# Optimization experiments

Measured on AMD Instinct MI355X. Metric: run time of the kernel, lower is better.

## Reference

```python
import jax, jax.numpy as jnp
import numpy as np

C = 64          # residual channels
N_LAYERS = 30
MAX_STEPS = 200
SQRT2 = 2.0 ** 0.5


def _conv1d(x, W, b, dilation=1, pad=0):
    # x: [B, Cin, T], W: [Cout, Cin, K], b: [Cout]
    y = jax.lax.conv_general_dilated(
        x, W, window_strides=(1,), padding=[(pad, pad)],
        rhs_dilation=(dilation,), dimension_numbers=('NCH', 'OIH', 'NCH'))
    return y + b[None, :, None]


def _silu(x):
    return x * jax.nn.sigmoid(x)


def _emb_table():
    steps = jnp.arange(MAX_STEPS, dtype=jnp.float32)[:, None]      # [200,1]
    dims = jnp.arange(64, dtype=jnp.float32)[None, :]              # [1,64]
    t = steps * 10.0 ** (dims * 4.0 / 63.0)                        # [200,64]
    return jnp.concatenate([jnp.sin(t), jnp.cos(t)], axis=1)       # [200,128]


def setup_inputs() -> dict:
    key = jax.random.key(0)
    ks = jax.random.split(key, 20)
    B, T = 4, 16384
    f32 = jnp.float32
    inp = {
        'audio': jax.random.normal(ks[0], (B, 1, T), dtype=f32),
        'diffusion_step': jax.random.randint(ks[1], (B,), 0, MAX_STEPS),
        # input projection Conv1d(1, 64, 1)
        'in_W': jax.random.normal(ks[2], (C, 1, 1), f32) * 1.0,
        'in_b': jax.random.normal(ks[3], (C,), f32) * 0.01,
        # diffusion embedding MLP 128->512->512
        'p1_W': jax.random.normal(ks[4], (512, 128), f32) * (1.0 / np.sqrt(128)),
        'p1_b': jnp.zeros((512,), f32),
        'p2_W': jax.random.normal(ks[5], (512, 512), f32) * (1.0 / np.sqrt(512)),
        'p2_b': jnp.zeros((512,), f32),
        # per-layer params (stacked over 30 layers)
        'dw_W': jax.random.normal(ks[6], (N_LAYERS, 2 * C, C, 3), f32) * (1.0 / np.sqrt(3 * C)),
        'dw_b': jnp.zeros((N_LAYERS, 2 * C), f32),
        'dp_W': jax.random.normal(ks[7], (N_LAYERS, C, 512), f32) * (1.0 / np.sqrt(512)),
        'dp_b': jnp.zeros((N_LAYERS, C), f32),
        'op_W': jax.random.normal(ks[8], (N_LAYERS, 2 * C, C, 1), f32) * (1.0 / np.sqrt(C)),
        'op_b': jnp.zeros((N_LAYERS, 2 * C), f32),
        # skip projection Conv1d(64,64,1)
        'sk_W': jax.random.normal(ks[9], (C, C, 1), f32) * (1.0 / np.sqrt(C)),
        'sk_b': jnp.zeros((C,), f32),
        # output projection Conv1d(64,1,1), weight zero-init like original
        'out_W': jnp.zeros((1, C, 1), f32),
        'out_b': jax.random.normal(ks[10], (1,), f32) * 0.01,
    }
    return inp


def reference(audio, diffusion_step, in_W, in_b, p1_W, p1_b, p2_W, p2_b,
              dw_W, dw_b, dp_W, dp_b, op_W, op_b, sk_W, sk_b, out_W, out_b):
    x = jax.nn.relu(_conv1d(audio, in_W, in_b))                    # [B,64,T]
    # diffusion embedding
    t = _emb_table()[diffusion_step]                               # [B,128]
    t = _silu(t @ p1_W.T + p1_b)                                   # [B,512]
    t = _silu(t @ p2_W.T + p2_b)                                   # [B,512]
    skip = None
    for i in range(N_LAYERS):
        d = 2 ** (i % 10)
        cond = (t @ dp_W[i].T + dp_b[i])[:, :, None]               # [B,64,1]
        y = _conv1d(x + cond, dw_W[i], dw_b[i], dilation=d, pad=d) # [B,128,T]
        gate, filt = y[:, :C], y[:, C:]
        y = jax.nn.sigmoid(gate) * jnp.tanh(filt)                  # [B,64,T]
        y = _conv1d(y, op_W[i], op_b[i])                           # [B,128,T]
        residual, sk = y[:, :C], y[:, C:]
        x = (x + residual) / SQRT2
        skip = sk if skip is None else skip + sk
    x = skip / np.sqrt(float(N_LAYERS)).astype(np.float32)
    x = jax.nn.relu(_conv1d(x, sk_W, sk_b))
    return _conv1d(x, out_W, out_b)                                # [B,1,T]
```

## Files before the change

### kernel.cpp

```cpp
#include <hip/hip_runtime.h>
#include <math.h>

#define C 64
#define NL 30
#define T 16384
#define B 4

typedef __bf16 bf16_t;
typedef __bf16 bf16x8 __attribute__((ext_vector_type(8)));
typedef __bf16 bf16x4 __attribute__((ext_vector_type(4)));
typedef float f32x4 __attribute__((ext_vector_type(4)));

typedef const __attribute__((address_space(1))) unsigned int glb_u32;
typedef __attribute__((address_space(3))) unsigned int lds_u32;

constexpr float INV_SQRT2   = 0.70710678118654752440f;
constexpr float INV_SQRT_NL = 0.18257418583505537115f;

__device__ __forceinline__ float fsig(float x) {
    return __builtin_amdgcn_rcpf(1.f + __builtin_amdgcn_exp2f(-1.44269504089f * x));
}
__device__ __forceinline__ float ftanh(float x) {
    return fmaf(2.f, __builtin_amdgcn_rcpf(1.f + __builtin_amdgcn_exp2f(-2.88539008178f * x)), -1.f);
}
__device__ __forceinline__ int swz(int off) { return off ^ ((off >> 3) & 0x70); }

__global__ void pack_weights(const float* __restrict__ dw_W,
                             const float* __restrict__ op_W,
                             const float* __restrict__ sk_W,
                             bf16_t* __restrict__ convpk,
                             bf16_t* __restrict__ oppk,
                             bf16_t* __restrict__ skpk) {
    int idx = blockIdx.x * 256 + threadIdx.x;
    const int ndw = NL * 128 * 192;
    const int nop = NL * 128 * 64;
    if (idx < ndw) {
        int k = idx % 192; int r = idx / 192;
        int oc = r % 128;  int l = r / 128;
        int tap = k >> 6, ic = k & 63;
        convpk[idx] = (bf16_t)dw_W[((l * 128 + oc) * 64 + ic) * 3 + tap];
    } else if (idx < ndw + nop) {
        oppk[idx - ndw] = (bf16_t)op_W[idx - ndw];
    } else if (idx < ndw + nop + 4096) {
        int j = idx - ndw - nop;
        skpk[j] = (bf16_t)(sk_W[j] * INV_SQRT_NL);
    }
}

__global__ void cond_embp1(const int* __restrict__ step,
                           const float* __restrict__ p1_W, const float* __restrict__ p1_b,
                           float* __restrict__ h1out) {
    __shared__ float e[128];
    __shared__ float red[256];
    int b = blockIdx.x, blk = blockIdx.y, tid = threadIdx.x;
    int s = step[b];
    if (tid < 128) {
        int d = tid & 63;
        float tf = (float)s * powf(10.f, (float)d * 4.f / 63.f);
        double td = (double)tf;
        e[tid] = (tid < 64) ? (float)sin(td) : (float)cos(td);
    }
    __syncthreads();
    int ol = tid >> 2, q = tid & 3;
    int o = blk * 64 + ol;
    const float4* wr = (const float4*)(p1_W + o * 128 + q * 32);
    const float4* ev = (const float4*)(e + q * 32);
    float a = 0.f;
    #pragma unroll
    for (int j = 0; j < 8; ++j) {
        float4 wv = wr[j]; float4 xv = ev[j];
        a = fmaf(wv.x, xv.x, a); a = fmaf(wv.y, xv.y, a);
        a = fmaf(wv.z, xv.z, a); a = fmaf(wv.w, xv.w, a);
    }
    red[tid] = a;
    __syncthreads();
    if (q == 0) {
        float v = red[tid] + red[tid + 1] + red[tid + 2] + red[tid + 3] + p1_b[o];
        h1out[b * 512 + o] = v / (1.f + expf(-v));
    }
}

__global__ void cond_p2(const float* __restrict__ h1,
                        const float* __restrict__ p2_W, const float* __restrict__ p2_b,
                        float* __restrict__ h2out) {
    __shared__ float red[256];
    int b = blockIdx.x, blk = blockIdx.y, tid = threadIdx.x;
    int ol = tid >> 2, q = tid & 3;
    int o = blk * 64 + ol;
    const float4* wr = (const float4*)(p2_W + o * 512 + q * 128);
    const float4* hv = (const float4*)(h1 + b * 512 + q * 128);
    float a = 0.f;
    #pragma unroll 8
    for (int j = 0; j < 32; ++j) {
        float4 wv = wr[j]; float4 xv = hv[j];
        a = fmaf(wv.x, xv.x, a); a = fmaf(wv.y, xv.y, a);
        a = fmaf(wv.z, xv.z, a); a = fmaf(wv.w, xv.w, a);
    }
    red[tid] = a;
    __syncthreads();
    if (q == 0) {
        float v = red[tid] + red[tid + 1] + red[tid + 2] + red[tid + 3] + p2_b[o];
        h2out[b * 512 + o] = v / (1.f + expf(-v));
    }
}

__global__ void cond_stage2b(const float* __restrict__ h2,
                             const float* __restrict__ dp_W, const float* __restrict__ dp_b,
                             const bf16_t* __restrict__ convpk,
                             const float* __restrict__ dw_b,
                             float* __restrict__ bias2) {
    __shared__ float red[256];
    __shared__ float cond_s[64];
    int l = blockIdx.x, b = blockIdx.y;
    int tid = threadIdx.x;
    {
        int o = tid >> 2, q = tid & 3;
        const float4* wr = (const float4*)(dp_W + ((size_t)l * C + o) * 512 + q * 128);
        const float4* h = (const float4*)(h2 + b * 512 + q * 128);
        float a = 0.f;
        #pragma unroll 8
        for (int j = 0; j < 32; ++j) {
            float4 wv = wr[j]; float4 hv = h[j];
            a = fmaf(wv.x, hv.x, a); a = fmaf(wv.y, hv.y, a);
            a = fmaf(wv.z, hv.z, a); a = fmaf(wv.w, hv.w, a);
        }
        red[tid] = a;
        __syncthreads();
        if (q == 0)
            cond_s[o] = red[tid] + red[tid + 1] + red[tid + 2] + red[tid + 3] + dp_b[l * C + o];
    }
    __syncthreads();
    int oc = tid & 127, kh = tid >> 7;
    const bf16_t* wr = convpk + ((size_t)l * 128 + oc) * 192 + kh * 96;
    float a = kh ? 0.f : dw_b[l * 128 + oc];
    #pragma unroll
    for (int j = 0; j < 96; ++j)
        a = fmaf((float)wr[j], cond_s[(kh * 96 + j) & 63], a);
    __syncthreads();
    red[tid] = a;
    __syncthreads();
    if (tid < 128)
        bias2[(l * B + b) * 128 + tid] = red[tid] + red[tid + 128];
}

__global__ void in_conv(const float* __restrict__ audio,
                        const float* __restrict__ in_W, const float* __restrict__ in_b,
                        bf16_t* __restrict__ x) {
    int idx = blockIdx.x * 256 + threadIdx.x;
    int cb = idx & 7;
    int t = (idx >> 3) & (T - 1);
    int b = idx >> 17;
    float av = audio[b * T + t];
    bf16x8 o;
    #pragma unroll
    for (int j = 0; j < 8; ++j) {
        int c = cb * 8 + j;
        o[j] = (bf16_t)fmaxf(fmaf(in_W[c], av, in_b[c]), 0.f);
    }
    *(bf16x8*)(x + ((size_t)b * T + t) * 64 + cb * 8) = o;
}

__global__ __launch_bounds__(256) void layer_kernel(
    const bf16_t* __restrict__ x_in, bf16_t* __restrict__ x_out, bf16_t* __restrict__ skip,
    const bf16_t* __restrict__ convpk, const bf16_t* __restrict__ oppk,
    const float* __restrict__ bias2, const float* __restrict__ op_b,
    const bf16_t* __restrict__ zpage,
    int layer, int dil, int first)
{
    __shared__ uint4 smem_u[2048];
    char* sm = (char*)smem_u;

    int tid = threadIdx.x;
    int w = __builtin_amdgcn_readfirstlane(tid >> 6);
    int l = tid & 63;
    int lr = l & 15;
    int g = l >> 4;
    int b = blockIdx.y;
    int bid = blockIdx.x;
    int tile = ((bid & 7) << 4) + (bid >> 3);
    int tbase = tile * 128;
    const bf16_t* xb = x_in + (size_t)b * T * 64;

    bf16x8 cA[2][6];
    const bf16_t* cw = convpk + (size_t)layer * 128 * 192;
    #pragma unroll
    for (int mf = 0; mf < 2; ++mf)
        #pragma unroll
        for (int kf = 0; kf < 6; ++kf)
            cA[mf][kf] = *(const bf16x8*)(cw + (mf * 64 + w * 16 + lr) * 192 + kf * 32 + g * 8);
    bf16x8 oA[2][2];
    const bf16_t* ow = oppk + (size_t)layer * 128 * 64;
    #pragma unroll
    for (int mf = 0; mf < 2; ++mf)
        #pragma unroll
        for (int kf = 0; kf < 2; ++kf)
            oA[mf][kf] = *(const bf16x8*)(ow + (mf * 64 + w * 16 + lr) * 64 + kf * 32 + g * 8);
    f32x4 bC[2], bO[2];
    const float* b2 = bias2 + (layer * B + b) * 128;
    const float* ob = op_b + layer * 2 * C;
    #pragma unroll
    for (int mf = 0; mf < 2; ++mf)
        #pragma unroll
        for (int r = 0; r < 4; ++r) {
            bC[mf][r] = b2[mf * 64 + w * 16 + g * 4 + r];
            bO[mf][r] = ob[mf * 64 + w * 16 + g * 4 + r];
        }

    size_t bb = (size_t)b * T * 64;

    for (int st = 0; st < 2; ++st) {
        int t0 = tbase + st * 64;

        #pragma unroll
        for (int it = 0; it < 6; ++it) {
            int qq = it * 256 + tid;
            int slice = qq >> 9, row = (qq >> 3) & 63, c16 = qq & 7;
            int ts = t0 + row + (slice - 1) * dil;
            int c16s = c16 ^ (row & 7);
            const bf16_t* src = ((unsigned)ts < (unsigned)T)
                ? (xb + (size_t)ts * 64 + c16s * 8)
                : (zpage + c16s * 8);
            __builtin_amdgcn_global_load_lds((glb_u32*)src,
                (lds_u32*)(sm + it * 4096 + w * 1024), 16, 0, 0);
        }
        __syncthreads();

        f32x4 acc[2][4];
        #pragma unroll
        for (int mf = 0; mf < 2; ++mf)
            #pragma unroll
            for (int nf = 0; nf < 4; ++nf) acc[mf][nf] = bC[mf];
        #pragma unroll
        for (int kf = 0; kf < 6; ++kf) {
            int tap = kf >> 1;
            int kc = (kf & 1) * 32;
            bf16x8 Bf[4];
            #pragma unroll
            for (int nf = 0; nf < 4; ++nf) {
                int off = tap * 8192 + (nf * 16 + lr) * 128 + (kc + g * 8) * 2;
                Bf[nf] = *(const bf16x8*)(sm + swz(off));
            }
            #pragma unroll
            for (int mf = 0; mf < 2; ++mf)
                #pragma unroll
                for (int nf = 0; nf < 4; ++nf)
                    acc[mf][nf] = __builtin_amdgcn_mfma_f32_16x16x32_bf16(
                        cA[mf][kf], Bf[nf], acc[mf][nf], 0, 0, 0);
        }

        #pragma unroll
        for (int nf = 0; nf < 4; ++nf) {
            union { bf16_t hh[4]; uint2 u; } zp;
            #pragma unroll
            for (int r = 0; r < 4; ++r)
                zp.hh[r] = (bf16_t)(fsig(acc[0][nf][r]) * ftanh(acc[1][nf][r]));
            int off = 24576 + (nf * 16 + lr) * 128 + (w * 16 + g * 4) * 2;
            *(uint2*)(sm + swz(off)) = zp.u;
        }
        __syncthreads();

        f32x4 acc2[2][4];
        #pragma unroll
        for (int mf = 0; mf < 2; ++mf)
            #pragma unroll
            for (int nf = 0; nf < 4; ++nf) acc2[mf][nf] = bO[mf];
        #pragma unroll
        for (int kf = 0; kf < 2; ++kf) {
            bf16x8 Zf[4];
            #pragma unroll
            for (int nf = 0; nf < 4; ++nf) {
                int off = 24576 + (nf * 16 + lr) * 128 + (kf * 32 + g * 8) * 2;
                Zf[nf] = *(const bf16x8*)(sm + swz(off));
            }
            #pragma unroll
            for (int mf = 0; mf < 2; ++mf)
                #pragma unroll
                for (int nf = 0; nf < 4; ++nf)
                    acc2[mf][nf] = __builtin_amdgcn_mfma_f32_16x16x32_bf16(
                        oA[mf][kf], Zf[nf], acc2[mf][nf], 0, 0, 0);
        }

        #pragma unroll
        for (int nf = 0; nf < 4; ++nf) {
            int t = t0 + nf * 16 + lr;
            int c0 = w * 16 + g * 4;
            int xoff = 8192 + (nf * 16 + lr) * 128 + c0 * 2;
            bf16x4 xv = *(const bf16x4*)(sm + swz(xoff));
            bf16x4 ro, so;
            bf16_t* sp = skip + bb + (size_t)t * 64 + c0;
            if (first) {
                #pragma unroll
                for (int r = 0; r < 4; ++r) {
                    ro[r] = (bf16_t)(((float)xv[r] + acc2[0][nf][r]) * INV_SQRT2);
                    so[r] = (bf16_t)acc2[1][nf][r];
                }
            } else {
                bf16x4 sv = *(const bf16x4*)sp;
                #pragma unroll
                for (int r = 0; r < 4; ++r) {
                    ro[r] = (bf16_t)(((float)xv[r] + acc2[0][nf][r]) * INV_SQRT2);
                    so[r] = (bf16_t)((float)sv[r] + acc2[1][nf][r]);
                }
            }
            *(bf16x4*)(x_out + bb + (size_t)t * 64 + c0) = ro;
            *(bf16x4*)sp = so;
        }
        if (st == 0) __syncthreads();
    }
}

template<int D1, int D2, int YOFF, int NYR, int XOFF, int NXR>
__global__ __launch_bounds__(256) void fused_pair(
    const bf16_t* __restrict__ x_in, bf16_t* __restrict__ x_out,
    bf16_t* __restrict__ skip,
    const bf16_t* __restrict__ convpk, const bf16_t* __restrict__ oppk,
    const float* __restrict__ bias2, const float* __restrict__ op_b,
    const bf16_t* __restrict__ zpage, int layerA, int first)
{
    extern __shared__ char sm[];
    constexpr int NYF = NYR / 16;
    constexpr int CF  = YOFF / 16;
    constexpr int YS  = NXR * 128;
    constexpr int ZS  = YS + NYR * 128;

    int tid = threadIdx.x;
    int w = __builtin_amdgcn_readfirstlane(tid >> 6);
    int l = tid & 63, lr = l & 15, g = l >> 4;
    int bid = blockIdx.x;
    int tile = ((bid & 7) << 5) + (bid >> 3);
    int b = blockIdx.y;
    int t0 = tile * 64;
    size_t bb = (size_t)b * T * 64;
    const bf16_t* xb = x_in + bb;
    int c0 = w * 16 + g * 4;

    #pragma unroll
    for (int r = 0; r < NXR / 32; ++r) {
        int row = r * 32 + (tid >> 3), c16 = tid & 7;
        int ts = t0 - XOFF + row;
        int c16s = c16 ^ (row & 7);
        const bf16_t* src = ((unsigned)ts < (unsigned)T)
            ? (xb + (size_t)ts * 64 + c16s * 8)
            : (zpage + c16s * 8);
        __builtin_amdgcn_global_load_lds((glb_u32*)src,
            (lds_u32*)(sm + r * 4096 + w * 1024), 16, 0, 0);
    }

    float skr[16];
    #pragma unroll
    for (int i = 0; i < 16; ++i) skr[i] = 0.f;

    bf16x8 cA[2][6];
    {
        const bf16_t* cw = convpk + (size_t)layerA * 128 * 192;
        #pragma unroll
        for (int mf = 0; mf < 2; ++mf)
            #pragma unroll
            for (int kf = 0; kf < 6; ++kf)
                cA[mf][kf] = *(const bf16x8*)(cw + (mf * 64 + w * 16 + lr) * 192 + kf * 32 + g * 8);
    }
    bf16x8 oA[2][2];
    {
        const bf16_t* ow = oppk + (size_t)layerA * 128 * 64;
        #pragma unroll
        for (int mf = 0; mf < 2; ++mf)
            #pragma unroll
            for (int kf = 0; kf < 2; ++kf)
                oA[mf][kf] = *(const bf16x8*)(ow + (mf * 64 + w * 16 + lr) * 64 + kf * 32 + g * 8);
    }
    f32x4 bC[2], bO[2];
    {
        const float* b2 = bias2 + (layerA * B + b) * 128;
        const float* ob = op_b + layerA * 2 * C;
        #pragma unroll
        for (int mf = 0; mf < 2; ++mf)
            #pragma unroll
            for (int r = 0; r < 4; ++r) {
                bC[mf][r] = b2[mf * 64 + c0 + r];
                bO[mf][r] = ob[mf * 64 + c0 + r];
            }
    }
    __syncthreads();

    f32x4 acc[2][NYF];
    #pragma unroll
    for (int mf = 0; mf < 2; ++mf)
        #pragma unroll
        for (int nf = 0; nf < NYF; ++nf) acc[mf][nf] = bC[mf];
    #pragma unroll
    for (int kf = 0; kf < 6; ++kf) {
        int tap = kf >> 1;
        int kc = (kf & 1) * 32;
        bf16x8 Bf[NYF];
        #pragma unroll
        for (int nf = 0; nf < NYF; ++nf) {
            int ix = (nf * 16 + lr) + (XOFF - YOFF) + (tap - 1) * D1;
            Bf[nf] = *(const bf16x8*)(sm + swz(ix * 128 + (kc + g * 8) * 2));
        }
        #pragma unroll
        for (int mf = 0; mf < 2; ++mf)
            #pragma unroll
            for (int nf = 0; nf < NYF; ++nf)
                acc[mf][nf] = __builtin_amdgcn_mfma_f32_16x16x32_bf16(
                    cA[mf][kf], Bf[nf], acc[mf][nf], 0, 0, 0);
    }

    #pragma unroll
    for (int nf = 0; nf < NYF; ++nf) {
        union { bf16_t hh[4]; uint2 u; } zp;
        #pragma unroll
        for (int r = 0; r < 4; ++r)
            zp.hh[r] = (bf16_t)(fsig(acc[0][nf][r]) * ftanh(acc[1][nf][r]));
        int off = ZS + (nf * 16 + lr) * 128 + c0 * 2;
        *(uint2*)(sm + swz(off)) = zp.u;
    }
    __syncthreads();

    {
        f32x4 acc2[2][NYF];
        #pragma unroll
        for (int mf = 0; mf < 2; ++mf)
            #pragma unroll
            for (int nf = 0; nf < NYF; ++nf) acc2[mf][nf] = bO[mf];
        #pragma unroll
        for (int kf = 0; kf < 2; ++kf) {
            bf16x8 Zf[NYF];
            #pragma unroll
            for (int nf = 0; nf < NYF; ++nf) {
                int off = ZS + (nf * 16 + lr) * 128 + (kf * 32 + g * 8) * 2;
                Zf[nf] = *(const bf16x8*)(sm + swz(off));
            }
            #pragma unroll
            for (int mf = 0; mf < 2; ++mf)
                #pragma unroll
                for (int nf = 0; nf < NYF; ++nf)
                    acc2[mf][nf] = __builtin_amdgcn_mfma_f32_16x16x32_bf16(
                        oA[mf][kf], Zf[nf], acc2[mf][nf], 0, 0, 0);
        }
        #pragma unroll
        for (int nf = 0; nf < NYF; ++nf) {
            int iy = nf * 16 + lr;
            int ta = t0 - YOFF + iy;
            bool inr = ((unsigned)ta < (unsigned)T);
            int ixc = iy + (XOFF - YOFF);
            bf16x4 xv = *(const bf16x4*)(sm + swz(ixc * 128 + c0 * 2));
            bf16x4 yo;
            #pragma unroll
            for (int r = 0; r < 4; ++r) {
                float yv = ((float)xv[r] + acc2[0][nf][r]) * INV_SQRT2;
                yo[r] = inr ? (bf16_t)yv : (bf16_t)0.f;
                if (nf >= CF && nf < CF + 4)
                    skr[(nf - CF) * 4 + r] += acc2[1][nf][r];
            }
            *(bf16x4*)(sm + swz(YS + iy * 128 + c0 * 2)) = yo;
        }
    }

    int layerB = layerA + 1;
    bf16x8 cB[2][6];
    {
        const bf16_t* cw = convpk + (size_t)layerB * 128 * 192;
        #pragma unroll
        for (int mf = 0; mf < 2; ++mf)
            #pragma unroll
            for (int kf = 0; kf < 6; ++kf)
                cB[mf][kf] = *(const bf16x8*)(cw + (mf * 64 + w * 16 + lr) * 192 + kf * 32 + g * 8);
    }
    bf16x8 oB[2][2];
    {
        const bf16_t* ow = oppk + (size_t)layerB * 128 * 64;
        #pragma unroll
        for (int mf = 0; mf < 2; ++mf)
            #pragma unroll
            for (int kf = 0; kf < 2; ++kf)
                oB[mf][kf] = *(const bf16x8*)(ow + (mf * 64 + w * 16 + lr) * 64 + kf * 32 + g * 8);
    }
    f32x4 bCB[2], bOB[2];
    {
        const float* b2 = bias2 + (layerB * B + b) * 128;
        const float* ob = op_b + layerB * 2 * C;
        #pragma unroll
        for (int mf = 0; mf < 2; ++mf)
            #pragma unroll
            for (int r = 0; r < 4; ++r) {
                bCB[mf][r] = b2[mf * 64 + c0 + r];
                bOB[mf][r] = ob[mf * 64 + c0 + r];
            }
    }
    __syncthreads();

    f32x4 accB[2][4];
    #pragma unroll
    for (int mf = 0; mf < 2; ++mf)
        #pragma unroll
        for (int nf = 0; nf < 4; ++nf) accB[mf][nf] = bCB[mf];
    #pragma unroll
    for (int kf = 0; kf < 6; ++kf) {
        int tap = kf >> 1;
        int kc = (kf & 1) * 32;
        bf16x8 Bf[4];
        #pragma unroll
        for (int nf = 0; nf < 4; ++nf) {
            int jy = (nf * 16 + lr) + YOFF + (tap - 1) * D2;
            Bf[nf] = *(const bf16x8*)(sm + swz(YS + jy * 128 + (kc + g * 8) * 2));
        }
        #pragma unroll
        for (int mf = 0; mf < 2; ++mf)
            #pragma unroll
            for (int nf = 0; nf < 4; ++nf)
                accB[mf][nf] = __builtin_amdgcn_mfma_f32_16x16x32_bf16(
                    cB[mf][kf], Bf[nf], accB[mf][nf], 0, 0, 0);
    }

    #pragma unroll
    for (int nf = 0; nf < 4; ++nf) {
        union { bf16_t hh[4]; uint2 u; } zp;
        #pragma unroll
        for (int r = 0; r < 4; ++r)
            zp.hh[r] = (bf16_t)(fsig(accB[0][nf][r]) * ftanh(accB[1][nf][r]));
        int off = ZS + (nf * 16 + lr) * 128 + c0 * 2;
        *(uint2*)(sm + swz(off)) = zp.u;
    }
    __syncthreads();

    f32x4 acc2B[2][4];
    #pragma unroll
    for (int mf = 0; mf < 2; ++mf)
        #pragma unroll
        for (int nf = 0; nf < 4; ++nf) acc2B[mf][nf] = bOB[mf];
    #pragma unroll
    for (int kf = 0; kf < 2; ++kf) {
        bf16x8 Zf[4];
        #pragma unroll
        for (int nf = 0; nf < 4; ++nf) {
            int off = ZS + (nf * 16 + lr) * 128 + (kf * 32 + g * 8) * 2;
            Zf[nf] = *(const bf16x8*)(sm + swz(off));
        }
        #pragma unroll
        for (int mf = 0; mf < 2; ++mf)
            #pragma unroll
            for (int nf = 0; nf < 4; ++nf)
                acc2B[mf][nf] = __builtin_amdgcn_mfma_f32_16x16x32_bf16(
                    oB[mf][kf], Zf[nf], acc2B[mf][nf], 0, 0, 0);
    }
    #pragma unroll
    for (int nf = 0; nf < 4; ++nf) {
        int it = nf * 16 + lr;
        int t = t0 + it;
        int jyc = it + YOFF;
        bf16x4 yv = *(const bf16x4*)(sm + swz(YS + jyc * 128 + c0 * 2));
        bf16x4 ro, so;
        bf16_t* sp = skip + bb + (size_t)t * 64 + c0;
        if (first) {
            #pragma unroll
            for (int r = 0; r < 4; ++r) {
                ro[r] = (bf16_t)(((float)yv[r] + acc2B[0][nf][r]) * INV_SQRT2);
                so[r] = (bf16_t)(skr[nf * 4 + r] + acc2B[1][nf][r]);
            }
        } else {
            bf16x4 sv = *(const bf16x4*)sp;
            #pragma unroll
            for (int r = 0; r < 4; ++r) {
                ro[r] = (bf16_t)(((float)yv[r] + acc2B[0][nf][r]) * INV_SQRT2);
                so[r] = (bf16_t)((float)sv[r] + skr[nf * 4 + r] + acc2B[1][nf][r]);
            }
        }
        *(bf16x4*)(x_out + bb + (size_t)t * 64 + c0) = ro;
        *(bf16x4*)sp = so;
    }
}

__global__ __launch_bounds__(256) void final_kernel(
    const bf16_t* __restrict__ skip, const bf16_t* __restrict__ skpk,
    const float* __restrict__ sk_b,
    const float* __restrict__ out_W, const float* __restrict__ out_b,
    float* __restrict__ out)
{
    __shared__ uint4 tile_u[512];
    __shared__ float part[16][66];
    unsigned char* sm = (unsigned char*)tile_u;
    int tid = threadIdx.x;
    int w = __builtin_amdgcn_readfirstlane(tid >> 6);
    int l = tid & 63, lr = l & 15, g = l >> 4;
    int bid = blockIdx.x;
    int tile = ((bid & 7) << 5) + (bid >> 3);
    int b = blockIdx.y, t0 = tile * 64;
    const bf16_t* sb = skip + (size_t)b * T * 64;

    #pragma unroll
    for (int it = 0; it < 2; ++it) {
        int q = it * 256 + tid;
        int row = q >> 3, c16 = q & 7;
        uint4 val = *(const uint4*)(sb + (size_t)(t0 + row) * 64 + c16 * 8);
        *(uint4*)(sm + swz(row * 128 + c16 * 16)) = val;
    }

    bf16x8 aS[2];
    #pragma unroll
    for (int kf = 0; kf < 2; ++kf)
        aS[kf] = *(const bf16x8*)(skpk + (w * 16 + lr) * 64 + kf * 32 + g * 8);
    f32x4 acc[4];
    #pragma unroll
    for (int nf = 0; nf < 4; ++nf)
        #pragma unroll
        for (int r = 0; r < 4; ++r) acc[nf][r] = sk_b[w * 16 + g * 4 + r];
    __syncthreads();

    #pragma unroll
    for (int kf = 0; kf < 2; ++kf) {
        bf16x8 Bf[4];
        #pragma unroll
        for (int nf = 0; nf < 4; ++nf) {
            int off = (nf * 16 + lr) * 128 + (kf * 32 + g * 8) * 2;
            Bf[nf] = *(const bf16x8*)(sm + swz(off));
        }
        #pragma unroll
        for (int nf = 0; nf < 4; ++nf)
            acc[nf] = __builtin_amdgcn_mfma_f32_16x16x32_bf16(aS[kf], Bf[nf], acc[nf], 0, 0, 0);
    }

    #pragma unroll
    for (int nf = 0; nf < 4; ++nf) {
        float o = 0.f;
        #pragma unroll
        for (int r = 0; r < 4; ++r)
            o = fmaf(out_W[w * 16 + g * 4 + r], fmaxf(acc[nf][r], 0.f), o);
        part[w * 4 + g][nf * 16 + lr] = o;
    }
    __syncthreads();
    if (tid < 64) {
        float o = out_b[0];
        #pragma unroll
        for (int j = 0; j < 16; ++j) o += part[j][tid];
        out[(size_t)b * T + t0 + tid] = o;
    }
}

extern "C" void kernel_launch(void* const* d_in, const int* in_sizes, int n_in,
                              void* d_out, int out_size, void* d_ws, size_t ws_size,
                              hipStream_t stream) {
    const float* audio = (const float*)d_in[0];
    const int*   dstep = (const int*)d_in[1];
    const float* in_W  = (const float*)d_in[2];
    const float* in_b  = (const float*)d_in[3];
    const float* p1_W  = (const float*)d_in[4];
    const float* p1_b  = (const float*)d_in[5];
    const float* p2_W  = (const float*)d_in[6];
    const float* p2_b  = (const float*)d_in[7];
    const float* dw_W  = (const float*)d_in[8];
    const float* dw_b  = (const float*)d_in[9];
    const float* dp_W  = (const float*)d_in[10];
    const float* dp_b  = (const float*)d_in[11];
    const float* op_W  = (const float*)d_in[12];
    const float* op_b  = (const float*)d_in[13];
    const float* sk_W  = (const float*)d_in[14];
    const float* sk_b  = (const float*)d_in[15];
    const float* out_W = (const float*)d_in[16];
    const float* out_b = (const float*)d_in[17];

    float* ws = (float*)d_ws;
    const size_t NXE = (size_t)B * T * 64;
    float* h1    = ws;
    float* h2    = h1 + B * 512;
    float* bias2 = h2 + B * 512;
    float* zpg   = bias2 + NL * B * 128;
    bf16_t* xA   = (bf16_t*)(zpg + 128);
    bf16_t* xB   = xA + NXE;
    bf16_t* skip = xB + NXE;
    bf16_t* convpk = skip + NXE;
    bf16_t* oppk   = convpk + (size_t)NL * 128 * 192;
    bf16_t* skpk   = oppk + (size_t)NL * 128 * 64;

    hipMemsetAsync(zpg, 0, 512, stream);
    hipLaunchKernelGGL(pack_weights, dim3(3856), dim3(256), 0, stream,
                       dw_W, op_W, sk_W, convpk, oppk, skpk);
    hipLaunchKernelGGL(cond_embp1, dim3(B, 8), dim3(256), 0, stream,
                       dstep, p1_W, p1_b, h1);
    hipLaunchKernelGGL(cond_p2, dim3(B, 8), dim3(256), 0, stream,
                       h1, p2_W, p2_b, h2);
    hipLaunchKernelGGL(cond_stage2b, dim3(NL, B), dim3(256), 0, stream,
                       h2, dp_W, dp_b, convpk, dw_b, bias2);
    hipLaunchKernelGGL(in_conv, dim3(B * T * 8 / 256), dim3(256), 0, stream,
                       audio, in_W, in_b, xA);

    bf16_t* bufs[2] = { xA, xB };
    int cur = 0;
    const bf16_t* zpgc = (const bf16_t*)zpg;
    for (int dec = 0; dec < 3; ++dec) {
        int base = dec * 10;
        hipLaunchKernelGGL((fused_pair<1, 2, 16, 96, 32, 128>),
                           dim3(T / 64, B), dim3(256), 40960, stream,
                           bufs[cur], bufs[cur ^ 1], skip, convpk, oppk,
                           bias2, op_b, zpgc, base + 0, (dec == 0) ? 1 : 0);
        cur ^= 1;
        hipLaunchKernelGGL((fused_pair<4, 8, 16, 96, 32, 128>),
                           dim3(T / 64, B), dim3(256), 40960, stream,
                           bufs[cur], bufs[cur ^ 1], skip, convpk, oppk,
                           bias2, op_b, zpgc, base + 2, 0);
        cur ^= 1;
        hipLaunchKernelGGL((fused_pair<16, 32, 32, 128, 48, 160>),
                           dim3(T / 64, B), dim3(256), 53248, stream,
                           bufs[cur], bufs[cur ^ 1], skip, convpk, oppk,
                           bias2, op_b, zpgc, base + 4, 0);
        cur ^= 1;
        for (int j = 6; j < 10; ++j) {
            int dil = 1 << j;
            hipLaunchKernelGGL(layer_kernel, dim3(T / 128, B), dim3(256), 0, stream,
                               bufs[cur], bufs[cur ^ 1], skip, convpk, oppk,
                               bias2, op_b, zpgc, base + j, dil, 0);
            cur ^= 1;
        }
    }
    hipLaunchKernelGGL(final_kernel, dim3(T / 64, B), dim3(256), 0, stream,
                       skip, skpk, sk_b, out_W, out_b, (float*)d_out);
}
```

Baseline: 467.7 us.

## Fuse input conv into first layer pair and retile single-layer kernel

```diff
diff --git a/kernel.cpp b/kernel.cpp
--- a/kernel.cpp
+++ b/kernel.cpp
@@ -143,24 +143,7 @@
         bias2[(l * B + b) * 128 + tid] = red[tid] + red[tid + 128];
 }
 
-__global__ void in_conv(const float* __restrict__ audio,
-                        const float* __restrict__ in_W, const float* __restrict__ in_b,
-                        bf16_t* __restrict__ x) {
-    int idx = blockIdx.x * 256 + threadIdx.x;
-    int cb = idx & 7;
-    int t = (idx >> 3) & (T - 1);
-    int b = idx >> 17;
-    float av = audio[b * T + t];
-    bf16x8 o;
-    #pragma unroll
-    for (int j = 0; j < 8; ++j) {
-        int c = cb * 8 + j;
-        o[j] = (bf16_t)fmaxf(fmaf(in_W[c], av, in_b[c]), 0.f);
-    }
-    *(bf16x8*)(x + ((size_t)b * T + t) * 64 + cb * 8) = o;
-}
-
-__global__ __launch_bounds__(256) void layer_kernel(
+__global__ __launch_bounds__(256, 4) void layer_kernel(
     const bf16_t* __restrict__ x_in, bf16_t* __restrict__ x_out, bf16_t* __restrict__ skip,
     const bf16_t* __restrict__ convpk, const bf16_t* __restrict__ oppk,
     const float* __restrict__ bias2, const float* __restrict__ op_b,
@@ -177,9 +160,23 @@
     int g = l >> 4;
     int b = blockIdx.y;
     int bid = blockIdx.x;
-    int tile = ((bid & 7) << 4) + (bid >> 3);
-    int tbase = tile * 128;
+    int tile = ((bid & 7) << 5) + (bid >> 3);
+    int t0 = tile * 64;
     const bf16_t* xb = x_in + (size_t)b * T * 64;
+    size_t bb = (size_t)b * T * 64;
+
+    #pragma unroll
+    for (int it = 0; it < 6; ++it) {
+        int qq = it * 256 + tid;
+        int slice = qq >> 9, row = (qq >> 3) & 63, c16 = qq & 7;
+        int ts = t0 + row + (slice - 1) * dil;
+        int c16s = c16 ^ (row & 7);
+        const bf16_t* src = ((unsigned)ts < (unsigned)T)
+            ? (xb + (size_t)ts * 64 + c16s * 8)
+            : (zpage + c16s * 8);
+        __builtin_amdgcn_global_load_lds((glb_u32*)src,
+            (lds_u32*)(sm + it * 4096 + w * 1024), 16, 0, 0);
+    }
 
     bf16x8 cA[2][6];
     const bf16_t* cw = convpk + (size_t)layer * 128 * 192;
@@ -188,6 +185,37 @@
         #pragma unroll
         for (int kf = 0; kf < 6; ++kf)
             cA[mf][kf] = *(const bf16x8*)(cw + (mf * 64 + w * 16 + lr) * 192 + kf * 32 + g * 8);
+    f32x4 bC[2];
+    const float* b2 = bias2 + (layer * B + b) * 128;
+    #pragma unroll
+    for (int mf = 0; mf < 2; ++mf)
+        #pragma unroll
+        for (int r = 0; r < 4; ++r) bC[mf][r] = b2[mf * 64 + w * 16 + g * 4 + r];
+    __syncthreads();
+
+    f32x4 acc[2][4];
+    #pragma unroll
+    for (int mf = 0; mf < 2; ++mf)
+        #pragma unroll
+        for (int nf = 0; nf < 4; ++nf) acc[mf][nf] = bC[mf];
+    #pragma unroll
+    for (int kf = 0; kf < 6; ++kf) {
+        int tap = kf >> 1;
+        int kc = (kf & 1) * 32;
+        bf16x8 Bf[4];
+        #pragma unroll
+        for (int nf = 0; nf < 4; ++nf) {
+            int off = tap * 8192 + (nf * 16 + lr) * 128 + (kc + g * 8) * 2;
+            Bf[nf] = *(const bf16x8*)(sm + swz(off));
+        }
+        #pragma unroll
+        for (int mf = 0; mf < 2; ++mf)
+            #pragma unroll
+            for (int nf = 0; nf < 4; ++nf)
+                acc[mf][nf] = __builtin_amdgcn_mfma_f32_16x16x32_bf16(
+                    cA[mf][kf], Bf[nf], acc[mf][nf], 0, 0, 0);
+    }
+
     bf16x8 oA[2][2];
     const bf16_t* ow = oppk + (size_t)layer * 128 * 64;
     #pragma unroll
@@ -195,127 +223,82 @@
         #pragma unroll
         for (int kf = 0; kf < 2; ++kf)
             oA[mf][kf] = *(const bf16x8*)(ow + (mf * 64 + w * 16 + lr) * 64 + kf * 32 + g * 8);
-    f32x4 bC[2], bO[2];
-    const float* b2 = bias2 + (layer * B + b) * 128;
+    f32x4 bO[2];
     const float* ob = op_b + layer * 2 * C;
     #pragma unroll
     for (int mf = 0; mf < 2; ++mf)
         #pragma unroll
-        for (int r = 0; r < 4; ++r) {
-            bC[mf][r] = b2[mf * 64 + w * 16 + g * 4 + r];
-            bO[mf][r] = ob[mf * 64 + w * 16 + g * 4 + r];
-        }
-
-    size_t bb = (size_t)b * T * 64;
-
-    for (int st = 0; st < 2; ++st) {
-        int t0 = tbase + st * 64;
-
-        #pragma unroll
-        for (int it = 0; it < 6; ++it) {
-            int qq = it * 256 + tid;
-            int slice = qq >> 9, row = (qq >> 3) & 63, c16 = qq & 7;
-            int ts = t0 + row + (slice - 1) * dil;
-            int c16s = c16 ^ (row & 7);
-            const bf16_t* src = ((unsigned)ts < (unsigned)T)
-                ? (xb + (size_t)ts * 64 + c16s * 8)
-                : (zpage + c16s * 8);
-            __builtin_amdgcn_global_load_lds((glb_u32*)src,
-                (lds_u32*)(sm + it * 4096 + w * 1024), 16, 0, 0);
-        }
-        __syncthreads();
-
-        f32x4 acc[2][4];
-        #pragma unroll
-        for (int mf = 0; mf < 2; ++mf)
-            #pragma unroll
-            for (int nf = 0; nf < 4; ++nf) acc[mf][nf] = bC[mf];
-        #pragma unroll
-        for (int kf = 0; kf < 6; ++kf) {
-            int tap = kf >> 1;
-            int kc = (kf & 1) * 32;
-            bf16x8 Bf[4];
-            #pragma unroll
-            for (int nf = 0; nf < 4; ++nf) {
-                int off = tap * 8192 + (nf * 16 + lr) * 128 + (kc + g * 8) * 2;
-                Bf[nf] = *(const bf16x8*)(sm + swz(off));
-            }
-            #pragma unroll
-            for (int mf = 0; mf < 2; ++mf)
-                #pragma unroll
-                for (int nf = 0; nf < 4; ++nf)
-                    acc[mf][nf] = __builtin_amdgcn_mfma_f32_16x16x32_bf16(
-                        cA[mf][kf], Bf[nf], acc[mf][nf], 0, 0, 0);
-        }
-
+        for (int r = 0; r < 4; ++r) bO[mf][r] = ob[mf * 64 + w * 16 + g * 4 + r];
+
+    #pragma unroll
+    for (int nf = 0; nf < 4; ++nf) {
+        union { bf16_t hh[4]; uint2 u; } zp;
+        #pragma unroll
+        for (int r = 0; r < 4; ++r)
+            zp.hh[r] = (bf16_t)(fsig(acc[0][nf][r]) * ftanh(acc[1][nf][r]));
+        int off = 24576 + (nf * 16 + lr) * 128 + (w * 16 + g * 4) * 2;
+        *(uint2*)(sm + swz(off)) = zp.u;
+    }
+    __syncthreads();
+
+    f32x4 acc2[2][4];
+    #pragma unroll
+    for (int mf = 0; mf < 2; ++mf)
+        #pragma unroll
+        for (int nf = 0; nf < 4; ++nf) acc2[mf][nf] = bO[mf];
+    #pragma unroll
+    for (int kf = 0; kf < 2; ++kf) {
+        bf16x8 Zf[4];
         #pragma unroll
         for (int nf = 0; nf < 4; ++nf) {
-            union { bf16_t hh[4]; uint2 u; } zp;
-            #pragma unroll
-            for (int r = 0; r < 4; ++r)
-                zp.hh[r] = (bf16_t)(fsig(acc[0][nf][r]) * ftanh(acc[1][nf][r]));
-            int off = 24576 + (nf * 16 + lr) * 128 + (w * 16 + g * 4) * 2;
-            *(uint2*)(sm + swz(off)) = zp.u;
-        }
-        __syncthreads();
-
-        f32x4 acc2[2][4];
-        #pragma unroll
-        for (int mf = 0; mf < 2; ++mf)
-            #pragma unroll
-            for (int nf = 0; nf < 4; ++nf) acc2[mf][nf] = bO[mf];
-        #pragma unroll
-        for (int kf = 0; kf < 2; ++kf) {
-            bf16x8 Zf[4];
-            #pragma unroll
-            for (int nf = 0; nf < 4; ++nf) {
-                int off = 24576 + (nf * 16 + lr) * 128 + (kf * 32 + g * 8) * 2;
-                Zf[nf] = *(const bf16x8*)(sm + swz(off));
-            }
-            #pragma unroll
-            for (int mf = 0; mf < 2; ++mf)
-                #pragma unroll
-                for (int nf = 0; nf < 4; ++nf)
-                    acc2[mf][nf] = __builtin_amdgcn_mfma_f32_16x16x32_bf16(
-                        oA[mf][kf], Zf[nf], acc2[mf][nf], 0, 0, 0);
-        }
-
-        #pragma unroll
-        for (int nf = 0; nf < 4; ++nf) {
-            int t = t0 + nf * 16 + lr;
-            int c0 = w * 16 + g * 4;
-            int xoff = 8192 + (nf * 16 + lr) * 128 + c0 * 2;
-            bf16x4 xv = *(const bf16x4*)(sm + swz(xoff));
-            bf16x4 ro, so;
-            bf16_t* sp = skip + bb + (size_t)t * 64 + c0;
-            if (first) {
-                #pragma unroll
-                for (int r = 0; r < 4; ++r) {
-                    ro[r] = (bf16_t)(((float)xv[r] + acc2[0][nf][r]) * INV_SQRT2);
-                    so[r] = (bf16_t)acc2[1][nf][r];
-                }
-            } else {
-                bf16x4 sv = *(const bf16x4*)sp;
-                #pragma unroll
-                for (int r = 0; r < 4; ++r) {
-                    ro[r] = (bf16_t)(((float)xv[r] + acc2[0][nf][r]) * INV_SQRT2);
-                    so[r] = (bf16_t)((float)sv[r] + acc2[1][nf][r]);
-                }
-            }
-            *(bf16x4*)(x_out + bb + (size_t)t * 64 + c0) = ro;
-            *(bf16x4*)sp = so;
-        }
-        if (st == 0) __syncthreads();
-    }
-}
-
-template<int D1, int D2, int YOFF, int NYR, int XOFF, int NXR>
+            int off = 24576 + (nf * 16 + lr) * 128 + (kf * 32 + g * 8) * 2;
+            Zf[nf] = *(const bf16x8*)(sm + swz(off));
+        }
+        #pragma unroll
+        for (int mf = 0; mf < 2; ++mf)
+            #pragma unroll
+            for (int nf = 0; nf < 4; ++nf)
+                acc2[mf][nf] = __builtin_amdgcn_mfma_f32_16x16x32_bf16(
+                    oA[mf][kf], Zf[nf], acc2[mf][nf], 0, 0, 0);
+    }
+
+    #pragma unroll
+    for (int nf = 0; nf < 4; ++nf) {
+        int t = t0 + nf * 16 + lr;
+        int c0 = w * 16 + g * 4;
+        int xoff = 8192 + (nf * 16 + lr) * 128 + c0 * 2;
+        bf16x4 xv = *(const bf16x4*)(sm + swz(xoff));
+        bf16x4 ro, so;
+        bf16_t* sp = skip + bb + (size_t)t * 64 + c0;
+        if (first) {
+            #pragma unroll
+            for (int r = 0; r < 4; ++r) {
+                ro[r] = (bf16_t)(((float)xv[r] + acc2[0][nf][r]) * INV_SQRT2);
+                so[r] = (bf16_t)acc2[1][nf][r];
+            }
+        } else {
+            bf16x4 sv = *(const bf16x4*)sp;
+            #pragma unroll
+            for (int r = 0; r < 4; ++r) {
+                ro[r] = (bf16_t)(((float)xv[r] + acc2[0][nf][r]) * INV_SQRT2);
+                so[r] = (bf16_t)((float)sv[r] + acc2[1][nf][r]);
+            }
+        }
+        *(bf16x4*)(x_out + bb + (size_t)t * 64 + c0) = ro;
+        *(bf16x4*)sp = so;
+    }
+}
+
+template<int D1, int D2, int YOFF, int NYR, int XOFF, int NXR, int FROMAUD>
 __global__ __launch_bounds__(256) void fused_pair(
     const bf16_t* __restrict__ x_in, bf16_t* __restrict__ x_out,
     bf16_t* __restrict__ skip,
     const bf16_t* __restrict__ convpk, const bf16_t* __restrict__ oppk,
     const float* __restrict__ bias2, const float* __restrict__ op_b,
-    const bf16_t* __restrict__ zpage, int layerA, int first)
+    const bf16_t* __restrict__ zpage,
+    const float* __restrict__ audio,
+    const float* __restrict__ in_W, const float* __restrict__ in_b,
+    int layerA, int first)
 {
     extern __shared__ char sm[];
     constexpr int NYF = NYR / 16;
@@ -334,16 +317,38 @@
     const bf16_t* xb = x_in + bb;
     int c0 = w * 16 + g * 4;
 
-    #pragma unroll
-    for (int r = 0; r < NXR / 32; ++r) {
-        int row = r * 32 + (tid >> 3), c16 = tid & 7;
-        int ts = t0 - XOFF + row;
-        int c16s = c16 ^ (row & 7);
-        const bf16_t* src = ((unsigned)ts < (unsigned)T)
-            ? (xb + (size_t)ts * 64 + c16s * 8)
-            : (zpage + c16s * 8);
-        __builtin_amdgcn_global_load_lds((glb_u32*)src,
-            (lds_u32*)(sm + r * 4096 + w * 1024), 16, 0, 0);
+    if constexpr (FROMAUD) {
+        #pragma unroll
+        for (int r = 0; r < NXR / 32; ++r) {
+            int q = r * 256 + tid;
+            int row = q >> 3, c16 = q & 7;
+            int ts = t0 - XOFF + row;
+            bf16x8 o;
+            if ((unsigned)ts < (unsigned)T) {
+                float av = audio[(size_t)b * T + ts];
+                #pragma unroll
+                for (int j = 0; j < 8; ++j) {
+                    int c = c16 * 8 + j;
+                    o[j] = (bf16_t)fmaxf(fmaf(in_W[c], av, in_b[c]), 0.f);
+                }
+            } else {
+                #pragma unroll
+                for (int j = 0; j < 8; ++j) o[j] = (bf16_t)0.f;
+            }
+            *(bf16x8*)(sm + swz(row * 128 + c16 * 16)) = o;
+        }
+    } else {
+        #pragma unroll
+        for (int r = 0; r < NXR / 32; ++r) {
+            int row = r * 32 + (tid >> 3), c16 = tid & 7;
+            int ts = t0 - XOFF + row;
+            int c16s = c16 ^ (row & 7);
+            const bf16_t* src = ((unsigned)ts < (unsigned)T)
+                ? (xb + (size_t)ts * 64 + c16s * 8)
+                : (zpage + c16s * 8);
+            __builtin_amdgcn_global_load_lds((glb_u32*)src,
+                (lds_u32*)(sm + r * 4096 + w * 1024), 16, 0, 0);
+        }
     }
 
     float skr[16];
@@ -680,32 +685,37 @@
                        h1, p2_W, p2_b, h2);
     hipLaunchKernelGGL(cond_stage2b, dim3(NL, B), dim3(256), 0, stream,
                        h2, dp_W, dp_b, convpk, dw_b, bias2);
-    hipLaunchKernelGGL(in_conv, dim3(B * T * 8 / 256), dim3(256), 0, stream,
-                       audio, in_W, in_b, xA);
 
     bf16_t* bufs[2] = { xA, xB };
     int cur = 0;
     const bf16_t* zpgc = (const bf16_t*)zpg;
     for (int dec = 0; dec < 3; ++dec) {
         int base = dec * 10;
-        hipLaunchKernelGGL((fused_pair<1, 2, 16, 96, 32, 128>),
+        if (dec == 0) {
+            hipLaunchKernelGGL((fused_pair<1, 2, 16, 96, 32, 128, 1>),
+                               dim3(T / 64, B), dim3(256), 40960, stream,
+                               bufs[cur], bufs[cur ^ 1], skip, convpk, oppk,
+                               bias2, op_b, zpgc, audio, in_W, in_b, 0, 1);
+        } else {
+            hipLaunchKernelGGL((fused_pair<1, 2, 16, 96, 32, 128, 0>),
+                               dim3(T / 64, B), dim3(256), 40960, stream,
+                               bufs[cur], bufs[cur ^ 1], skip, convpk, oppk,
+                               bias2, op_b, zpgc, audio, in_W, in_b, base + 0, 0);
+        }
+        cur ^= 1;
+        hipLaunchKernelGGL((fused_pair<4, 8, 16, 96, 32, 128, 0>),
                            dim3(T / 64, B), dim3(256), 40960, stream,
                            bufs[cur], bufs[cur ^ 1], skip, convpk, oppk,
-                           bias2, op_b, zpgc, base + 0, (dec == 0) ? 1 : 0);
+                           bias2, op_b, zpgc, audio, in_W, in_b, base + 2, 0);
         cur ^= 1;
-        hipLaunchKernelGGL((fused_pair<4, 8, 16, 96, 32, 128>),
-                           dim3(T / 64, B), dim3(256), 40960, stream,
-                           bufs[cur], bufs[cur ^ 1], skip, convpk, oppk,
-                           bias2, op_b, zpgc, base + 2, 0);
-        cur ^= 1;
-        hipLaunchKernelGGL((fused_pair<16, 32, 32, 128, 48, 160>),
+        hipLaunchKernelGGL((fused_pair<16, 32, 32, 128, 48, 160, 0>),
                            dim3(T / 64, B), dim3(256), 53248, stream,
                            bufs[cur], bufs[cur ^ 1], skip, convpk, oppk,
-                           bias2, op_b, zpgc, base + 4, 0);
+                           bias2, op_b, zpgc, audio, in_W, in_b, base + 4, 0);
         cur ^= 1;
         for (int j = 6; j < 10; ++j) {
             int dil = 1 << j;
-            hipLaunchKernelGGL(layer_kernel, dim3(T / 128, B), dim3(256), 0, stream,
+            hipLaunchKernelGGL(layer_kernel, dim3(T / 64, B), dim3(256), 0, stream,
                                bufs[cur], bufs[cur ^ 1], skip, convpk, oppk,
                                bias2, op_b, zpgc, base + j, dil, 0);
             cur ^= 1;
```

Measured after the change: 484.9 us. +3.7%, slower.
